# Optimization experiments

Measured on AMD Instinct MI355X. Metric: run time of the kernel, lower is better.

Reference implementation:

```python
import jax, jax.numpy as jnp
import numpy as np

CUTOFF = 5.0

def ssp(x):
    # shifted softplus: ln(0.5*e^x + 0.5)
    return jax.nn.softplus(x) - jnp.log(2.0).astype(x.dtype)

def cosine_cutoff(r):
    return 0.5 * (jnp.cos(jnp.pi * r / CUTOFF) + 1.0) * (r < CUTOFF).astype(r.dtype)

def setup_inputs() -> dict:
    key = jax.random.key(0)
    ks = jax.random.split(key, 16)
    B, A, N, Nd, F, Din, Dout, Th = 2, 512, 1024, 64, 64, 128, 128, 25
    inp = {}
    inp['x'] = jax.random.normal(ks[0], (B, A, Din), dtype=jnp.float32)
    inp['r_double'] = jax.random.uniform(ks[1], (B, A, Nd), dtype=jnp.float32)
    inp['r_ij'] = jax.random.uniform(ks[2], (B, A, N), dtype=jnp.float32)
    inp['r_ik'] = jax.random.uniform(ks[3], (B, A, N), dtype=jnp.float32)
    inp['r_jk'] = jax.random.uniform(ks[4], (B, A, N), dtype=jnp.float32)
    inp['neighbors'] = jax.random.randint(ks[5], (B, A, Nd), 0, A, dtype=jnp.int32)
    inp['neighbor_mask'] = jnp.ones((B, A, Nd), dtype=jnp.float32)
    inp['neighbors_j'] = jax.random.randint(ks[6], (B, A, N), 0, A, dtype=jnp.int32)
    inp['neighbors_k'] = jax.random.randint(ks[7], (B, A, N), 0, A, dtype=jnp.int32)
    inp['triple_masks'] = jnp.ones((B, A, N), dtype=jnp.float32)
    inp['d_ijk'] = jax.random.uniform(ks[8], (B, A, N, Th), dtype=jnp.float32)
    s = 0.1
    inp['W_in2f'] = s * jax.random.normal(ks[9], (Din, F), dtype=jnp.float32)
    inp['W_t1'] = s * jax.random.normal(ks[10], (Th, F), dtype=jnp.float32)
    inp['b_t1'] = jnp.zeros((F,), dtype=jnp.float32)
    inp['W_t2'] = s * jax.random.normal(ks[11], (F, F), dtype=jnp.float32)
    inp['b_t2'] = jnp.zeros((F,), dtype=jnp.float32)
    inp['W_f2out'] = s * jax.random.normal(ks[12], (F, Dout), dtype=jnp.float32)
    inp['b_f2out'] = jnp.zeros((Dout,), dtype=jnp.float32)
    return inp

def reference(x, r_double, r_ij, r_ik, r_jk, neighbors, neighbor_mask,
              neighbors_j, neighbors_k, triple_masks, d_ijk,
              W_in2f, W_t1, b_t1, W_t2, b_t2, W_f2out, b_f2out):
    # Triple filter: 2-layer MLP on angular basis, modulated by cutoffs
    h = ssp(jnp.einsum('bant,tf->banf', d_ijk, W_t1) + b_t1)
    W_triple = jnp.einsum('banf,fg->bang', h, W_t2) + b_t2
    W_triple = W_triple * cosine_cutoff(r_ij)[..., None] * cosine_cutoff(r_ik)[..., None]

    # in2f: (B, A, F)
    y = jnp.einsum('bad,df->baf', x, W_in2f)
    B, A, N = neighbors_j.shape
    F = y.shape[-1]
    # gather neighbor features along atom axis
    yj = jnp.take_along_axis(y, neighbors_j.reshape(B, A * N, 1), axis=1).reshape(B, A, N, F)
    yk = jnp.take_along_axis(y, neighbors_k.reshape(B, A * N, 1), axis=1).reshape(B, A, N, F)
    w_ij = r_ij[..., None]
    w_ik = r_ik[..., None]
    y = (w_ij * yj + w_ik * yk) / (w_ij + w_ik)
    # filter multiply + masked sum aggregation over triples axis
    y = y * W_triple
    y = jnp.sum(y * triple_masks[..., None], axis=2)
    # f2out with shifted-softplus activation
    out = ssp(jnp.einsum('baf,fo->bao', y, W_f2out) + b_f2out)
    return out
```

## Files before the change

kernel.cpp:

```cpp
#include <hip/hip_runtime.h>
#include <hip/hip_fp16.h>

#define BB 2
#define AA 512
#define NN 1024
#define FF 64
#define DIN 128
#define DOUT 128
#define TH 25
#define ASTRIDE 40
#define HSTRIDE 72
#define NSPLIT 2
#define NIT 8

typedef _Float16 half8 __attribute__((ext_vector_type(8)));
typedef _Float16 half4v __attribute__((ext_vector_type(4)));
typedef float floatx4 __attribute__((ext_vector_type(4)));

#define LOG2E 1.44269504088896f
#define LN2F  0.693147180559945f

__device__ __forceinline__ float ssp_f(float x) {
    return __logf(0.5f * __expf(x) + 0.5f);
}

__device__ __forceinline__ float cutcos(float r) {
    float c = 0.5f * (__cosf(r * (3.14159265358979323846f / 5.0f)) + 1.0f);
    return (r < 5.0f) ? c : 0.0f;
}

__device__ __forceinline__ __half2 ssp2f(__half2 z) {
    const __half2 hlf = __float2half2_rn(0.5f);
    return h2log2(__hadd2(h2exp2(z), hlf));
}

__device__ __forceinline__ __half2 pk2(float a, float b) {
    auto v = __builtin_amdgcn_cvt_pkrtz(a, b);
    __half2 r;
    __builtin_memcpy(&r, &v, sizeof(r));
    return r;
}

__device__ __forceinline__ half4v pack4(__half2 lo, __half2 hi) {
    half4v r;
    __builtin_memcpy(&r, &lo, 4);
    __builtin_memcpy(reinterpret_cast<char*>(&r) + 4, &hi, 4);
    return r;
}

#define OFF_Y       0
#define OFF_PARTIAL (OFF_Y + (size_t)BB * AA * FF * 2)
#define OFF_B1      (OFF_PARTIAL + (size_t)NSPLIT * BB * AA * FF * 4)
#define OFF_B2      (OFF_B1 + 4 * 64 * 8 * 2)
#define OFF_BP      (OFF_B2 + 8 * 64 * 8 * 2)

__global__ void in2f_prep_kernel(const float* __restrict__ x,
                                 const float* __restrict__ Wi,
                                 _Float16* __restrict__ y,
                                 const float* __restrict__ W_t1, const float* __restrict__ b_t1,
                                 const float* __restrict__ W_t2, const float* __restrict__ b_t2,
                                 _Float16* __restrict__ B1tab, _Float16* __restrict__ B2tab,
                                 _Float16* __restrict__ BPtab) {
    __shared__ float xs[DIN];
    const int ba = blockIdx.x;
    const int t = threadIdx.x;
    xs[t] = x[ba * DIN + t];
    xs[t + 64] = x[ba * DIN + 64 + t];
    __syncthreads();
    float acc = 0.f;
#pragma unroll 8
    for (int d = 0; d < DIN; ++d) acc += xs[d] * Wi[d * FF + t];
    y[ba * FF + t] = (_Float16)acc;

    if (ba == 0) {
        const int lane = t, quad = t >> 4, l16 = t & 15;
#pragma unroll
        for (int g = 0; g < 4; ++g) {
            const int featA = g * 16 + l16;
#pragma unroll
            for (int j = 0; j < 8; ++j) {
                int k = quad * 8 + j;
                _Float16 v;
                if (k < TH)       v = (_Float16)(W_t1[k * FF + featA] * LOG2E);
                else if (k == TH) v = (_Float16)(b_t1[featA] * LOG2E - 1.0f);
                else              v = (_Float16)0.f;
                B1tab[(g * 64 + lane) * 8 + j] = v;
            }
#pragma unroll
            for (int e = 0; e < 2; ++e) {
                BPtab[((g * 2 + e) * 64 + lane) * 2 + 0] =
                    (_Float16)b_t2[g * 16 + quad * 4 + 2 * e];
                BPtab[((g * 2 + e) * 64 + lane) * 2 + 1] =
                    (_Float16)b_t2[g * 16 + quad * 4 + 2 * e + 1];
            }
#pragma unroll
            for (int q = 0; q < 2; ++q)
#pragma unroll
                for (int j = 0; j < 8; ++j)
                    B2tab[((g * 2 + q) * 64 + lane) * 8 + j] =
                        (_Float16)(W_t2[(q * 32 + quad * 8 + j) * FF + g * 16 + l16] * LN2F);
        }
    }
}

__global__ __launch_bounds__(256) void triple_kernel(
    const int* __restrict__ nbrj, const int* __restrict__ nbrk,
    const float* __restrict__ r_ij, const float* __restrict__ r_ik,
    const float* __restrict__ tmask, const float* __restrict__ d_ijk,
    const _Float16* __restrict__ B1tab, const _Float16* __restrict__ B2tab,
    const _Float16* __restrict__ BPtab,
    const _Float16* __restrict__ y_tab, float* __restrict__ partial) {

    __shared__ __align__(16) _Float16 a_tile[4][16 * ASTRIDE];
    __shared__ __align__(16) _Float16 h_tile[4][16 * HSTRIDE];
    __shared__ float red[4][FF];

    const int blk = blockIdx.x;
    const int ba = blk >> 1;
    const int split = blk & 1;
    const int b = ba >> 9;
    const int tid = threadIdx.x;
    const int w = tid >> 6;
    const int lane = tid & 63;
    const int quad = lane >> 4;
    const int l16 = lane & 15;
    const int rA = lane >> 3;
    const int fc = (lane & 7) * 8;

    const long ban = (long)ba * NN;
    const float* dbase = d_ijk + (long)ba * NN * TH;
    const _Float16* yb = y_tab + (long)b * (AA * FF);

    half8 B1[4];
    half8 B2[4][2];
    __half2 b2p[4][2];
#pragma unroll
    for (int g = 0; g < 4; ++g) {
        B1[g] = *(const half8*)(B1tab + (g * 64 + lane) * 8);
        B2[g][0] = *(const half8*)(B2tab + ((g * 2 + 0) * 64 + lane) * 8);
        B2[g][1] = *(const half8*)(B2tab + ((g * 2 + 1) * 64 + lane) * 8);
#pragma unroll
        for (int e = 0; e < 2; ++e)
            b2p[g][e] = *(const __half2*)(BPtab + ((g * 2 + e) * 64 + lane) * 2);
    }

    const int tile0 = split * 32 + quad * 4 + w;
    const long n0a = ban + (long)tile0 * 16 + l16;
    const long n1a = n0a + 256;
    const float rij0 = r_ij[n0a], rik0 = r_ik[n0a];
    const float rij1 = r_ij[n1a], rik1 = r_ik[n1a];
    const float iv0 = cutcos(rij0) * cutcos(rik0) * tmask[n0a] / (rij0 + rik0);
    const float iv1 = cutcos(rij1) * cutcos(rik1) * tmask[n1a] / (rij1 + rik1);
    const float wjL0 = rij0 * iv0, wkL0 = rik0 * iv0;
    const float wjL1 = rij1 * iv1, wkL1 = rik1 * iv1;
    const int pjL0 = nbrj[n0a], pkL0 = nbrk[n0a];
    const int pjL1 = nbrj[n1a], pkL1 = nbrk[n1a];

    for (int idx = lane; idx < 16 * 7; idx += 64) {
        int r = idx / 7, c = 25 + idx % 7;
        a_tile[w][r * ASTRIDE + c] = (c == 25) ? (_Float16)1.f : (_Float16)0.f;
    }

    int lofs2[3][2];
#pragma unroll
    for (int m = 0; m < 3; ++m)
#pragma unroll
        for (int e = 0; e < 2; ++e) {
            int s = m * 128 + lane * 2 + e;
            int r = s / TH, c = s - r * TH;
            lofs2[m][e] = r * ASTRIDE + c;
        }
    const int tofs = 15 * ASTRIDE + 9 + lane;

    float acc[8];
#pragma unroll
    for (int i = 0; i < 8; ++i) acc[i] = 0.f;
    const floatx4 zero4 = {0.f, 0.f, 0.f, 0.f};

    float2 pA[3];
    float pT = 0.f;
    const float* dp0 = dbase + (long)(split * 32 + w) * 16 * TH;
    {
#pragma unroll
        for (int m = 0; m < 3; ++m) pA[m] = *(const float2*)(dp0 + m * 128 + lane * 2);
        if (lane < 16) pT = dp0[384 + lane];
    }

#pragma unroll 1
    for (int it = 0; it < NIT; ++it) {
        const bool s1 = (it >= 4);
        const int sl0 = (it & 3) * 16 + rA;
        const int sl1 = sl0 + 8;
        const int pjS = s1 ? pjL1 : pjL0, pkS = s1 ? pkL1 : pkL0;
        const float wjS = s1 ? wjL1 : wjL0, wkS = s1 ? wkL1 : wkL0;
        const int pj0 = __shfl(pjS, sl0), pk0 = __shfl(pkS, sl0);
        const int pj1 = __shfl(pjS, sl1), pk1 = __shfl(pkS, sl1);
        half8 gj0 = *(const half8*)(yb + pj0 * FF + fc);
        half8 gk0 = *(const half8*)(yb + pk0 * FF + fc);
        half8 gj1 = *(const half8*)(yb + pj1 * FF + fc);
        half8 gk1 = *(const half8*)(yb + pk1 * FF + fc);

#pragma unroll
        for (int m = 0; m < 3; ++m) {
            a_tile[w][lofs2[m][0]] = (_Float16)pA[m].x;
            a_tile[w][lofs2[m][1]] = (_Float16)pA[m].y;
        }
        if (lane < 16) a_tile[w][tofs] = (_Float16)pT;

        if (it + 1 < NIT) {
            const float* dn = dp0 + (it + 1) * 1600;
#pragma unroll
            for (int m = 0; m < 3; ++m) pA[m] = *(const float2*)(dn + m * 128 + lane * 2);
            if (lane < 16) pT = dn[384 + lane];
        }

        const __half2 wj0 = __float2half2_rn(__shfl(wjS, sl0));
        const __half2 wk0 = __float2half2_rn(__shfl(wkS, sl0));
        const __half2 wj1 = __float2half2_rn(__shfl(wjS, sl1));
        const __half2 wk1 = __float2half2_rn(__shfl(wkS, sl1));

        half8 afrag = *(const half8*)&a_tile[w][l16 * ASTRIDE + quad * 8];
#pragma unroll
        for (int g = 0; g < 4; ++g) {
            floatx4 hv = __builtin_amdgcn_mfma_f32_16x16x32_f16(B1[g], afrag, zero4, 0, 0, 0);
            __half2 h01 = ssp2f(pk2(hv[0], hv[1]));
            __half2 h23 = ssp2f(pk2(hv[2], hv[3]));
            *(half4v*)&h_tile[w][l16 * HSTRIDE + g * 16 + quad * 4] = pack4(h01, h23);
        }

        half8 a2q0 = *(const half8*)&h_tile[w][l16 * HSTRIDE + quad * 8];
        half8 a2q1 = *(const half8*)&h_tile[w][l16 * HSTRIDE + 32 + quad * 8];
#pragma unroll
        for (int g = 0; g < 4; ++g) {
            floatx4 w2 = __builtin_amdgcn_mfma_f32_16x16x32_f16(B2[g][0], a2q0, zero4, 0, 0, 0);
            w2 = __builtin_amdgcn_mfma_f32_16x16x32_f16(B2[g][1], a2q1, w2, 0, 0, 0);
            __half2 f01 = __hadd2(pk2(w2[0], w2[1]), b2p[g][0]);
            __half2 f23 = __hadd2(pk2(w2[2], w2[3]), b2p[g][1]);
            *(half4v*)&h_tile[w][l16 * HSTRIDE + g * 16 + quad * 4] = pack4(f01, f23);
        }
        half8 f0 = *(const half8*)&h_tile[w][rA * HSTRIDE + fc];
        half8 f1 = *(const half8*)&h_tile[w][(8 + rA) * HSTRIDE + fc];

        const __half2* gj0p = (const __half2*)&gj0;
        const __half2* gk0p = (const __half2*)&gk0;
        const __half2* gj1p = (const __half2*)&gj1;
        const __half2* gk1p = (const __half2*)&gk1;
        const __half2* f0p = (const __half2*)&f0;
        const __half2* f1p = (const __half2*)&f1;
#pragma unroll
        for (int p = 0; p < 4; ++p) {
            __half2 fv0 = __hfma2(wj0, gj0p[p], __hmul2(wk0, gk0p[p]));
            __half2 fv1 = __hfma2(wj1, gj1p[p], __hmul2(wk1, gk1p[p]));
            __half2 tot = __hfma2(f1p[p], fv1, __hmul2(f0p[p], fv0));
            acc[2 * p]     += __low2float(tot);
            acc[2 * p + 1] += __high2float(tot);
        }
    }

#pragma unroll
    for (int i = 0; i < 8; ++i) {
        acc[i] += __shfl_xor(acc[i], 8, 64);
        acc[i] += __shfl_xor(acc[i], 16, 64);
        acc[i] += __shfl_xor(acc[i], 32, 64);
    }
    if (lane < 8)
#pragma unroll
        for (int i = 0; i < 8; ++i) red[w][lane * 8 + i] = acc[i];
    __syncthreads();

    if (tid < FF)
        partial[(split * (BB * AA) + ba) * FF + tid] =
            red[0][tid] + red[1][tid] + red[2][tid] + red[3][tid];
}

__global__ void out_kernel(const float* __restrict__ partial,
                           const float* __restrict__ Wf,
                           const float* __restrict__ bf,
                           float* __restrict__ out) {
    __shared__ float yag[FF];
    const int ba = blockIdx.x;
    const int t = threadIdx.x;
    if (t < FF) {
        float s = 0.f;
#pragma unroll
        for (int sp = 0; sp < NSPLIT; ++sp)
            s += partial[(sp * (BB * AA) + ba) * FF + t];
        yag[t] = s;
    }
    __syncthreads();
    float a = bf[t];
#pragma unroll 8
    for (int f = 0; f < FF; ++f) a += yag[f] * Wf[f * DOUT + t];
    out[(long)ba * DOUT + t] = ssp_f(a);
}

extern "C" void kernel_launch(void* const* d_in, const int* in_sizes, int n_in,
                              void* d_out, int out_size, void* d_ws, size_t ws_size,
                              hipStream_t stream) {
    const float* x       = (const float*)d_in[0];
    const float* r_ij    = (const float*)d_in[2];
    const float* r_ik    = (const float*)d_in[3];
    const int*   nbrj    = (const int*)d_in[7];
    const int*   nbrk    = (const int*)d_in[8];
    const float* tmask   = (const float*)d_in[9];
    const float* d_ijk   = (const float*)d_in[10];
    const float* W_in2f  = (const float*)d_in[11];
    const float* W_t1    = (const float*)d_in[12];
    const float* b_t1    = (const float*)d_in[13];
    const float* W_t2    = (const float*)d_in[14];
    const float* b_t2    = (const float*)d_in[15];
    const float* W_f2out = (const float*)d_in[16];
    const float* b_f2out = (const float*)d_in[17];
    float* out = (float*)d_out;

    char* ws = (char*)d_ws;
    _Float16* y      = (_Float16*)(ws + OFF_Y);
    float* partial   = (float*)(ws + OFF_PARTIAL);
    _Float16* B1tab  = (_Float16*)(ws + OFF_B1);
    _Float16* B2tab  = (_Float16*)(ws + OFF_B2);
    _Float16* BPtab  = (_Float16*)(ws + OFF_BP);

    in2f_prep_kernel<<<BB * AA, 64, 0, stream>>>(x, W_in2f, y, W_t1, b_t1,
                                                 W_t2, b_t2, B1tab, B2tab, BPtab);
    triple_kernel<<<BB * AA * NSPLIT, 256, 0, stream>>>(nbrj, nbrk, r_ij, r_ik,
                                                        tmask, d_ijk, B1tab, B2tab,
                                                        BPtab, y, partial);
    out_kernel<<<BB * AA, 128, 0, stream>>>(partial, W_f2out, b_f2out, out);
}
```

Measured before the change: 234.0 us.

## Cut VGPR pressure: pack neighbor indices and weights, reload W_t2 fragments per iteration

Stops holding the second-layer weight fragments (32 VGPRs) in registers for the whole kernel. They are now reloaded from global memory (expected to hit cache) inside each loop iteration, and an empty asm barrier stops the compiler from hoisting those loads back out. Neighbor j/k indices are packed into one 16-bit pair and the two interpolation weights into a half2, which halves the shuffles and the live registers. The aim is lower register pressure for better occupancy, at the cost of extra per-iteration loads and fp16 weight rounding done earlier.

```diff
diff --git a/kernel.cpp b/kernel.cpp
--- a/kernel.cpp
+++ b/kernel.cpp
@@ -132,29 +132,32 @@
     const _Float16* yb = y_tab + (long)b * (AA * FF);
 
     half8 B1[4];
-    half8 B2[4][2];
     __half2 b2p[4][2];
 #pragma unroll
     for (int g = 0; g < 4; ++g) {
         B1[g] = *(const half8*)(B1tab + (g * 64 + lane) * 8);
-        B2[g][0] = *(const half8*)(B2tab + ((g * 2 + 0) * 64 + lane) * 8);
-        B2[g][1] = *(const half8*)(B2tab + ((g * 2 + 1) * 64 + lane) * 8);
 #pragma unroll
         for (int e = 0; e < 2; ++e)
             b2p[g][e] = *(const __half2*)(BPtab + ((g * 2 + e) * 64 + lane) * 2);
     }
+    const _Float16* b2gp = B2tab + lane * 8;
 
     const int tile0 = split * 32 + quad * 4 + w;
     const long n0a = ban + (long)tile0 * 16 + l16;
     const long n1a = n0a + 256;
-    const float rij0 = r_ij[n0a], rik0 = r_ik[n0a];
-    const float rij1 = r_ij[n1a], rik1 = r_ik[n1a];
-    const float iv0 = cutcos(rij0) * cutcos(rik0) * tmask[n0a] / (rij0 + rik0);
-    const float iv1 = cutcos(rij1) * cutcos(rik1) * tmask[n1a] / (rij1 + rik1);
-    const float wjL0 = rij0 * iv0, wkL0 = rik0 * iv0;
-    const float wjL1 = rij1 * iv1, wkL1 = rik1 * iv1;
-    const int pjL0 = nbrj[n0a], pkL0 = nbrk[n0a];
-    const int pjL1 = nbrj[n1a], pkL1 = nbrk[n1a];
+    int pp0, pp1, wp0, wp1;
+    {
+        const float rij0 = r_ij[n0a], rik0 = r_ik[n0a];
+        const float rij1 = r_ij[n1a], rik1 = r_ik[n1a];
+        const float iv0 = cutcos(rij0) * cutcos(rik0) * tmask[n0a] / (rij0 + rik0);
+        const float iv1 = cutcos(rij1) * cutcos(rik1) * tmask[n1a] / (rij1 + rik1);
+        __half2 w0 = pk2(rij0 * iv0, rik0 * iv0);
+        __half2 w1 = pk2(rij1 * iv1, rik1 * iv1);
+        __builtin_memcpy(&wp0, &w0, 4);
+        __builtin_memcpy(&wp1, &w1, 4);
+        pp0 = nbrj[n0a] | (nbrk[n0a] << 16);
+        pp1 = nbrj[n1a] | (nbrk[n1a] << 16);
+    }
 
     for (int idx = lane; idx < 16 * 7; idx += 64) {
         int r = idx / 7, c = 25 + idx % 7;
@@ -191,10 +194,12 @@
         const bool s1 = (it >= 4);
         const int sl0 = (it & 3) * 16 + rA;
         const int sl1 = sl0 + 8;
-        const int pjS = s1 ? pjL1 : pjL0, pkS = s1 ? pkL1 : pkL0;
-        const float wjS = s1 ? wjL1 : wjL0, wkS = s1 ? wkL1 : wkL0;
-        const int pj0 = __shfl(pjS, sl0), pk0 = __shfl(pkS, sl0);
-        const int pj1 = __shfl(pjS, sl1), pk1 = __shfl(pkS, sl1);
+        const int ppS = s1 ? pp1 : pp0;
+        const int wpS = s1 ? wp1 : wp0;
+        const int ppa = __shfl(ppS, sl0), ppb = __shfl(ppS, sl1);
+        const int wpa = __shfl(wpS, sl0), wpb = __shfl(wpS, sl1);
+        const int pj0 = ppa & 0xffff, pk0 = ((unsigned)ppa) >> 16;
+        const int pj1 = ppb & 0xffff, pk1 = ((unsigned)ppb) >> 16;
         half8 gj0 = *(const half8*)(yb + pj0 * FF + fc);
         half8 gk0 = *(const half8*)(yb + pk0 * FF + fc);
         half8 gj1 = *(const half8*)(yb + pj1 * FF + fc);
@@ -214,10 +219,13 @@
             if (lane < 16) pT = dn[384 + lane];
         }
 
-        const __half2 wj0 = __float2half2_rn(__shfl(wjS, sl0));
-        const __half2 wk0 = __float2half2_rn(__shfl(wkS, sl0));
-        const __half2 wj1 = __float2half2_rn(__shfl(wjS, sl1));
-        const __half2 wk1 = __float2half2_rn(__shfl(wkS, sl1));
+        __half2 wv0, wv1;
+        __builtin_memcpy(&wv0, &wpa, 4);
+        __builtin_memcpy(&wv1, &wpb, 4);
+        const __half2 wj0 = __half2half2(__low2half(wv0));
+        const __half2 wk0 = __half2half2(__high2half(wv0));
+        const __half2 wj1 = __half2half2(__low2half(wv1));
+        const __half2 wk1 = __half2half2(__high2half(wv1));
 
         half8 afrag = *(const half8*)&a_tile[w][l16 * ASTRIDE + quad * 8];
 #pragma unroll
@@ -232,8 +240,12 @@
         half8 a2q1 = *(const half8*)&h_tile[w][l16 * HSTRIDE + 32 + quad * 8];
 #pragma unroll
         for (int g = 0; g < 4; ++g) {
-            floatx4 w2 = __builtin_amdgcn_mfma_f32_16x16x32_f16(B2[g][0], a2q0, zero4, 0, 0, 0);
-            w2 = __builtin_amdgcn_mfma_f32_16x16x32_f16(B2[g][1], a2q1, w2, 0, 0, 0);
+            const _Float16* b2it = b2gp;
+            asm volatile("" : "+v"(b2it));
+            half8 B2g0 = *(const half8*)(b2it + (g * 2 + 0) * 512);
+            half8 B2g1 = *(const half8*)(b2it + (g * 2 + 1) * 512);
+            floatx4 w2 = __builtin_amdgcn_mfma_f32_16x16x32_f16(B2g0, a2q0, zero4, 0, 0, 0);
+            w2 = __builtin_amdgcn_mfma_f32_16x16x32_f16(B2g1, a2q1, w2, 0, 0, 0);
             __half2 f01 = __hadd2(pk2(w2[0], w2[1]), b2p[g][0]);
             __half2 f23 = __hadd2(pk2(w2[2], w2[3]), b2p[g][1]);
             *(half4v*)&h_tile[w][l16 * HSTRIDE + g * 16 + quad * 4] = pack4(f01, f23);
```

Result: slower. 249.2 us (+6.5%).
